# Performance work log

Measured on AMD Instinct MI355X. Metric: run time of the kernel, lower is better.

## Reference

```python
import jax, jax.numpy as jnp
import numpy as np

INPUT_DIM = 6
HIDDEN = 128


def neighbor_mean(x, adj):
    # x: [B,N,F], adj: [B,N,N]; node i averages itself + neighbors (adj>0)
    mask = (adj > 0).astype(x.dtype)  # [B,N,N]
    s = jnp.einsum('bij,bjf->bif', mask, x) + x  # sum neighbors + self
    cnt = mask.sum(-1) + 1.0  # [B,N]
    return s / cnt[..., None]


def lstm_scan(x, Wi, Wh, bi, bh, reverse=False):
    # x: [B,T,F]; Wi: [4H,F]; Wh: [4H,H]; gate order i,f,g,o (torch)
    B, T, F = x.shape
    H = Wh.shape[1]
    xw = jnp.einsum('btf,gf->btg', x, Wi) + bi + bh  # [B,T,4H]
    def step(carry, xt):
        h, c = carry
        z = xt + h @ Wh.T  # [B,4H]
        i, f, g, o = jnp.split(z, 4, axis=-1)
        i = jax.nn.sigmoid(i); f = jax.nn.sigmoid(f)
        g = jnp.tanh(g); o = jax.nn.sigmoid(o)
        c = f * c + i * g
        h = o * jnp.tanh(c)
        return (h, c), h
    init = (jnp.zeros((B, H), x.dtype), jnp.zeros((B, H), x.dtype))
    xs = jnp.swapaxes(xw, 0, 1)  # [T,B,4H]
    (hT, cT), hs = jax.lax.scan(step, init, xs, reverse=reverse)
    return hT


def setup_inputs():
    key = jax.random.key(0)
    ks = jax.random.split(key, 12)
    B, N = 4096, 64
    inp = {
        'device_idx': jax.random.uniform(ks[0], (B,), jnp.float32),
        'matrix': jax.random.uniform(ks[1], (B, N, N), jnp.float32),
        'features': jax.random.normal(ks[2], (B, N, INPUT_DIM), jnp.float32),
    }
    s = 1.0 / np.sqrt(HIDDEN)
    def u(k, shape):
        return jax.random.uniform(k, shape, jnp.float32, -s, s)
    inp['Wi_f'] = u(ks[3], (4 * HIDDEN, INPUT_DIM))
    inp['Wh_f'] = u(ks[4], (4 * HIDDEN, HIDDEN))
    inp['bi_f'] = u(ks[5], (4 * HIDDEN,))
    inp['bh_f'] = u(ks[6], (4 * HIDDEN,))
    inp['Wi_b'] = u(ks[7], (4 * HIDDEN, INPUT_DIM))
    inp['Wh_b'] = u(ks[8], (4 * HIDDEN, HIDDEN))
    inp['bi_b'] = u(ks[9], (4 * HIDDEN,))
    inp['bh_b'] = u(ks[10], (4 * HIDDEN,))
    inp['fc_w'] = u(ks[11], (1, 2 * HIDDEN + 1))
    inp['fc_b'] = jnp.zeros((1,), jnp.float32)
    return inp


def reference(device_idx, matrix, features, Wi_f, Wh_f, bi_f, bh_f, Wi_b, Wh_b, bi_b, bh_b, fc_w, fc_b):
    upd = neighbor_mean(features, matrix)  # [B,N,6]
    h_fwd = lstm_scan(upd, Wi_f, Wh_f, bi_f, bh_f, reverse=False)  # [B,H]
    h_bwd = lstm_scan(upd, Wi_b, Wh_b, bi_b, bh_b, reverse=True)   # [B,H]
    hn = jnp.concatenate([h_fwd, h_bwd], axis=1)  # [B,2H]
    final = jnp.concatenate([device_idx[:, None], hn], axis=1)  # [B,2H+1]
    y = final @ fc_w.T + fc_b
    return y.reshape(-1)
```

## Files before the change

kernel.cpp:

```cpp
#include <hip/hip_runtime.h>
#include <hip/hip_bf16.h>

#define B_TOTAL 4096
#define LOG2E 1.44269504088896f

typedef short short8 __attribute__((ext_vector_type(8)));
typedef float f32x4 __attribute__((ext_vector_type(4)));
typedef int   i32x4 __attribute__((ext_vector_type(4)));

__device__ __forceinline__ unsigned short rne_bf16(float x) {
    unsigned int u = __float_as_uint(x);
    unsigned int r = (u + 0x7fffu + ((u >> 16) & 1u)) >> 16;
    return (unsigned short)r;
}
__device__ __forceinline__ unsigned int cvt2bf(float lo, float hi) {
    unsigned int r;
    asm("v_cvt_pk_bf16_f32 %0, %1, %2" : "=v"(r) : "v"(lo), "v"(hi));
    return r;
}

__global__ __launch_bounds__(256) void k_neighbor_mean(
    const float* __restrict__ matrix,
    const float* __restrict__ features,
    float* __restrict__ upd)
{
    __shared__ float adj[64][65];
    __shared__ float fx[64][6];
    const int b = blockIdx.x;
    const int tid = threadIdx.x;
    const float* mb_ = matrix + (size_t)b * 4096;
    for (int idx = tid; idx < 4096; idx += 256) adj[idx >> 6][idx & 63] = mb_[idx];
    const float* fb = features + (size_t)b * 384;
    for (int idx = tid; idx < 384; idx += 256) fx[idx / 6][idx % 6] = fb[idx];
    __syncthreads();
    if (tid < 64) {
        const int i = tid;
        float s0=0,s1=0,s2=0,s3=0,s4=0,s5=0,cnt=0;
        for (int j = 0; j < 64; j++) {
            float m = adj[i][j] > 0.0f ? 1.0f : 0.0f;
            cnt += m;
            s0 += m*fx[j][0]; s1 += m*fx[j][1]; s2 += m*fx[j][2];
            s3 += m*fx[j][3]; s4 += m*fx[j][4]; s5 += m*fx[j][5];
        }
        const float inv = 1.0f / (cnt + 1.0f);
        float* o = upd + (size_t)b * 384 + i * 6;
        o[0]=(s0+fx[i][0])*inv; o[1]=(s1+fx[i][1])*inv; o[2]=(s2+fx[i][2])*inv;
        o[3]=(s3+fx[i][3])*inv; o[4]=(s4+fx[i][4])*inv; o[5]=(s5+fx[i][5])*inv;
    }
}

__global__ __launch_bounds__(256) void k_wprep5(
    const float* __restrict__ Wi_f, const float* __restrict__ Wh_f,
    const float* __restrict__ bi_f, const float* __restrict__ bh_f,
    const float* __restrict__ Wi_b, const float* __restrict__ Wh_b,
    const float* __restrict__ bi_b, const float* __restrict__ bh_b,
    signed char* __restrict__ Wd1, signed char* __restrict__ Wd2,
    unsigned short* __restrict__ AwU, float* __restrict__ BqO)
{
    const int idx = blockIdx.x * 256 + threadIdx.x;
    if (idx < 131072) {
        const int dir = idx >> 16;
        const int r = idx & 65535;
        const int mtg = r >> 11;
        const int kc  = (r >> 10) & 1;
        const int l   = (r >> 4) & 63;
        const int e   = r & 15;
        const int n = mtg * 16 + (l & 15);
        const int j = ((n & 3) << 7) + (n >> 2);
        const int ks = kc * 64 + 16 * (l >> 4) + e;
        const int hu = 8 * (ks >> 3) + 4 * (ks & 1) + ((ks & 7) >> 1);
        const float w = (dir ? Wh_b : Wh_f)[j * 128 + hu];
        const float a = w * (512.0f * LOG2E);
        const float r1 = rintf(a);
        Wd1[idx] = (signed char)(int)r1;
        Wd2[idx] = (signed char)(int)rintf((a - r1) * 128.0f);
    } else if (idx < 163840) {
        const int i2 = idx - 131072;
        const int dir = i2 >> 14;
        const int r = i2 & 16383;
        const int mtg = r >> 9, l = (r >> 3) & 63, e = r & 7;
        const int n = mtg * 16 + (l & 15);
        const int j = ((n & 3) << 7) + (n >> 2);
        const float sc = ((n & 3) == 2) ? 2.0f * LOG2E : LOG2E;
        float w = 0.0f;
        if ((l >> 4) == 0 && e < 6) w = (dir ? Wi_b : Wi_f)[j * 6 + e] * sc;
        AwU[i2] = rne_bf16(w);
    } else if (idx < 164864) {
        const int i2 = idx - 163840;
        const int dir = i2 >> 9;
        const int n = i2 & 511;
        const int j = ((n & 3) << 7) + (n >> 2);
        const float sc = ((n & 3) == 2) ? 2.0f * LOG2E : LOG2E;
        BqO[i2] = ((dir ? bi_b : bi_f)[j] + (dir ? bh_b : bh_f)[j]) * sc;
    }
}

__global__ __launch_bounds__(1024) void k_lstm8(
    const float* __restrict__ upd,
    const signed char* __restrict__ Wd1,
    const signed char* __restrict__ Wd2,
    const unsigned short* __restrict__ AwU,
    const float* __restrict__ Bq,
    float* __restrict__ hout)
{
    __shared__ i32x4 HsV[2048];
    __shared__ i32x4 UsV[2048];
    char* Hb = (char*)HsV;
    char* Ub = (char*)UsV;
    const int tid  = threadIdx.x;
    const int wave = tid >> 6;
    const int lane = tid & 63;
    const int dir  = blockIdx.y;
    const int b0   = blockIdx.x * 32;
    const int l15  = lane & 15;
    const int lhi  = lane >> 4;
    const int hu0  = 8 * wave + lhi, hu1 = hu0 + 4;

    i32x4 wd1[2][2], wd2[2][2];
    short8 awu[2];
    f32x4 bias[2];
    #pragma unroll
    for (int mt = 0; mt < 2; mt++) {
        const int mtg = 2 * wave + mt;
        #pragma unroll
        for (int kc = 0; kc < 2; kc++) {
            wd1[mt][kc] = *(const i32x4*)(Wd1 + dir * 65536 + mtg * 2048 + kc * 1024 + lane * 16);
            wd2[mt][kc] = *(const i32x4*)(Wd2 + dir * 65536 + mtg * 2048 + kc * 1024 + lane * 16);
        }
        awu[mt]  = *(const short8*)(AwU + dir * 16384 + mtg * 512 + lane * 8);
        bias[mt] = *(const f32x4*)(Bq + dir * 512 + mtg * 16 + 4 * lhi);
    }

    for (int i = tid; i < 2048; i += 1024) {
        const int t = i >> 5, b = i & 31;
        const float2* p = (const float2*)(upd + (size_t)(b0 + b) * 384 + t * 6);
        const float2 a0 = p[0], a1 = p[1], a2 = p[2];
        i32x4 v;
        v[0] = (int)cvt2bf(a0.x, a0.y);
        v[1] = (int)cvt2bf(a1.x, a1.y);
        v[2] = (int)cvt2bf(a2.x, a2.y);
        v[3] = 0;
        *(i32x4*)(Ub + (b >> 4) * 16384 + t * 256 + (b & 15) * 16) = v;
    }
    for (int i = tid; i < 8192; i += 1024) ((int*)Hb)[i] = 0;

    int ra[2], wa[2];
    #pragma unroll
    for (int g = 0; g < 2; g++) {
        ra[g] = g * 16384 + 4096 + l15 * 144 + lhi * 16;
        wa[g] = g * 16384 + l15 * 144 + 8 * wave + 2 * lhi;
    }
    float cs[2][2] = {{0.0f, 0.0f}, {0.0f, 0.0f}};
    f32x4 Ua[2][2];
    i32x4 Aa[2][2], Ba[2][2];
    __syncthreads();

    const i32x4 zi = {0, 0, 0, 0};

    {
        const int tt = dir ? 63 : 0;
        const short8 fu = *(const short8*)(Ub + tt * 256 + l15 * 16);
        const i32x4 h1k0 = *(const i32x4*)(Hb + ra[0]);
        const i32x4 h1k1 = *(const i32x4*)(Hb + ra[0] + 64);
        const i32x4 h2k0 = *(const i32x4*)(Hb + ra[0] + 8192);
        const i32x4 h2k1 = *(const i32x4*)(Hb + ra[0] + 8256);
        ra[0] ^= 0x1000;
        #pragma unroll
        for (int mt = 0; mt < 2; mt++) {
            Ua[0][mt] = __builtin_amdgcn_mfma_f32_16x16x32_bf16(awu[mt], fu, bias[mt], 0, 0, 0);
            i32x4 a = __builtin_amdgcn_mfma_i32_16x16x64_i8(wd1[mt][0], h1k0, zi, 0, 0, 0);
            a = __builtin_amdgcn_mfma_i32_16x16x64_i8(wd1[mt][1], h1k1, a, 0, 0, 0);
            i32x4 b = __builtin_amdgcn_mfma_i32_16x16x64_i8(wd1[mt][0], h2k0, zi, 0, 0, 0);
            b = __builtin_amdgcn_mfma_i32_16x16x64_i8(wd1[mt][1], h2k1, b, 0, 0, 0);
            b = __builtin_amdgcn_mfma_i32_16x16x64_i8(wd2[mt][0], h1k0, b, 0, 0, 0);
            b = __builtin_amdgcn_mfma_i32_16x16x64_i8(wd2[mt][1], h1k1, b, 0, 0, 0);
            Aa[0][mt] = a; Ba[0][mt] = b;
        }
    }

    #pragma unroll 2
    for (int iv = 0; iv < 128; ++iv) {
        const int gc = iv & 1;
        const int sc = iv >> 1;

        float z[2][4];
        #pragma unroll
        for (int mt = 0; mt < 2; mt++)
            #pragma unroll
            for (int i = 0; i < 4; i++) {
                const int T = (Aa[gc][mt][i] << 7) + Ba[gc][mt][i];
                z[mt][i] = fmaf((float)T, (i == 2) ? 0x1p-21f : 0x1p-22f, Ua[gc][mt][i]);
            }

        if (iv < 127) {
            const int gi = gc ^ 1;
            const int si = (iv + 1) >> 1;
            const int tt = dir ? (63 - si) : si;
            const short8 fu = *(const short8*)(Ub + gi * 16384 + tt * 256 + l15 * 16);
            const i32x4 h1k0 = *(const i32x4*)(Hb + ra[gi]);
            const i32x4 h1k1 = *(const i32x4*)(Hb + ra[gi] + 64);
            const i32x4 h2k0 = *(const i32x4*)(Hb + ra[gi] + 8192);
            const i32x4 h2k1 = *(const i32x4*)(Hb + ra[gi] + 8256);
            ra[gi] ^= 0x1000;
            __builtin_amdgcn_s_setprio(1);
            #pragma unroll
            for (int mt = 0; mt < 2; mt++) {
                Ua[gi][mt] = __builtin_amdgcn_mfma_f32_16x16x32_bf16(awu[mt], fu, bias[mt], 0, 0, 0);
                i32x4 a = __builtin_amdgcn_mfma_i32_16x16x64_i8(wd1[mt][0], h1k0, zi, 0, 0, 0);
                a = __builtin_amdgcn_mfma_i32_16x16x64_i8(wd1[mt][1], h1k1, a, 0, 0, 0);
                i32x4 b = __builtin_amdgcn_mfma_i32_16x16x64_i8(wd1[mt][0], h2k0, zi, 0, 0, 0);
                b = __builtin_amdgcn_mfma_i32_16x16x64_i8(wd1[mt][1], h2k1, b, 0, 0, 0);
                b = __builtin_amdgcn_mfma_i32_16x16x64_i8(wd2[mt][0], h1k0, b, 0, 0, 0);
                b = __builtin_amdgcn_mfma_i32_16x16x64_i8(wd2[mt][1], h1k1, b, 0, 0, 0);
                Aa[gi][mt] = a; Ba[gi][mt] = b;
            }
            __builtin_amdgcn_s_setprio(0);
        }

        float ig[2], fg[2], gg[2], og[2], Dq[2], hh[2];
        #pragma unroll
        for (int mt = 0; mt < 2; mt++) {
            const float D0 = 1.0f + __builtin_amdgcn_exp2f(-z[mt][0]);
            const float D1 = 1.0f + __builtin_amdgcn_exp2f(-z[mt][1]);
            const float D2 = 1.0f + __builtin_amdgcn_exp2f( z[mt][2]);
            const float D3 = 1.0f + __builtin_amdgcn_exp2f(-z[mt][3]);
            const float P2 = D0 * D1, P3 = P2 * D2, P4 = P3 * D3;
            const float r  = __builtin_amdgcn_rcpf(P4);
            const float Q2 = D3 * D2, Q3 = Q2 * D1;
            ig[mt] = r * Q3;
            fg[mt] = (r * Q2) * D0;
            og[mt] = r * P3;
            gg[mt] = fmaf(-2.0f, (r * P2) * D3, 1.0f);
        }
        #pragma unroll
        for (int mt = 0; mt < 2; mt++) {
            cs[gc][mt] = fmaf(fg[mt], cs[gc][mt], ig[mt] * gg[mt]);
            Dq[mt] = 1.0f + __builtin_amdgcn_exp2f(fminf(cs[gc][mt] * (2.0f * LOG2E), 30.0f));
        }
        const float rq = __builtin_amdgcn_rcpf(Dq[0] * Dq[1]);
        hh[0] = og[0] * fmaf(-2.0f, rq * Dq[1], 1.0f);
        hh[1] = og[1] * fmaf(-2.0f, rq * Dq[0], 1.0f);

        if (sc < 63) {
            int d1[2], d2[2];
            #pragma unroll
            for (int mt = 0; mt < 2; mt++) {
                const int t = __float_as_int(fmaf(hh[mt], 8192.0f, 12582912.0f)) - 0x4B400000;
                d1[mt] = (t + 64) >> 7;
                d2[mt] = t - (d1[mt] << 7);
            }
            *(unsigned short*)(Hb + wa[gc]) =
                (unsigned short)__builtin_amdgcn_perm((unsigned)d1[1], (unsigned)d1[0], 0x0400);
            *(unsigned short*)(Hb + wa[gc] + 8192) =
                (unsigned short)__builtin_amdgcn_perm((unsigned)d2[1], (unsigned)d2[0], 0x0400);
        } else {
            float* o = hout + ((size_t)dir * B_TOTAL + b0 + gc * 16 + l15) * 128;
            o[hu0] = hh[0];
            o[hu1] = hh[1];
        }
        wa[gc] ^= 0x1000;
        __syncthreads();
    }
}

__global__ __launch_bounds__(256) void k_final(
    const float* __restrict__ hout,
    const float* __restrict__ device_idx,
    const float* __restrict__ fc_w,
    const float* __restrict__ fc_b,
    float* __restrict__ y)
{
    const int wave = threadIdx.x >> 6;
    const int lane = threadIdx.x & 63;
    const int b = blockIdx.x * 4 + wave;
    const float* hf = hout + (size_t)b * 128;
    const float* hb = hout + ((size_t)B_TOTAL + b) * 128;
    float p = fc_w[1 + lane]        * hf[lane]
            + fc_w[1 + 64 + lane]   * hf[64 + lane]
            + fc_w[129 + lane]      * hb[lane]
            + fc_w[129 + 64 + lane] * hb[64 + lane];
    #pragma unroll
    for (int off = 32; off; off >>= 1) p += __shfl_xor(p, off, 64);
    if (lane == 0) y[b] = p + fc_w[0] * device_idx[b] + fc_b[0];
}

extern "C" void kernel_launch(void* const* d_in, const int* in_sizes, int n_in,
                              void* d_out, int out_size, void* d_ws, size_t ws_size,
                              hipStream_t stream) {
    const float* device_idx = (const float*)d_in[0];
    const float* matrix     = (const float*)d_in[1];
    const float* features   = (const float*)d_in[2];
    const float* Wi_f = (const float*)d_in[3];
    const float* Wh_f = (const float*)d_in[4];
    const float* bi_f = (const float*)d_in[5];
    const float* bh_f = (const float*)d_in[6];
    const float* Wi_b = (const float*)d_in[7];
    const float* Wh_b = (const float*)d_in[8];
    const float* bi_b = (const float*)d_in[9];
    const float* bh_b = (const float*)d_in[10];
    const float* fc_w = (const float*)d_in[11];
    const float* fc_b = (const float*)d_in[12];
    float* out = (float*)d_out;

    float* ws = (float*)d_ws;
    float*          upd  = ws;
    signed char*    Wd1  = (signed char*)(ws + 1572864);
    signed char*    Wd2  = (signed char*)(ws + 1605632);
    unsigned short* AwU  = (unsigned short*)(ws + 1638400);
    float*          Bq   = ws + 1654784;
    float*          hout = ws + 1655808;

    hipLaunchKernelGGL(k_neighbor_mean, dim3(B_TOTAL), dim3(256), 0, stream,
                       matrix, features, upd);
    hipLaunchKernelGGL(k_wprep5, dim3(644), dim3(256), 0, stream,
                       Wi_f, Wh_f, bi_f, bh_f, Wi_b, Wh_b, bi_b, bh_b,
                       Wd1, Wd2, AwU, Bq);
    hipLaunchKernelGGL(k_lstm8, dim3(B_TOTAL / 32, 2), dim3(1024), 0, stream,
                       upd, Wd1, Wd2, AwU, Bq, hout);
    hipLaunchKernelGGL(k_final, dim3(B_TOTAL / 4), dim3(256), 0, stream,
                       hout, device_idx, fc_w, fc_b, out);
}
```

Measured before the change: 163.2 us.

## Process 16 batch rows per LSTM block without two-group interleave, use packed float2 math

The LSTM kernel previously gave each 1024-thread block 32 batch rows as two 16-row groups. It interleaved them so one group's MFMA work overlapped the other group's gate math. Now each block handles 16 rows in a simple per-step loop, which doubles the grid (512 blocks) and halves LDS use. The gate and cell math is also rewritten in f32x2 vectors to encourage packed FP32 ops. This trades the intra-block MFMA/VALU overlap for more blocks per CU and lower register and LDS pressure, relying on the hardware to overlap work across blocks instead.

```diff
diff --git a/kernel.cpp b/kernel.cpp
--- a/kernel.cpp
+++ b/kernel.cpp
@@ -6,6 +6,7 @@
 
 typedef short short8 __attribute__((ext_vector_type(8)));
 typedef float f32x4 __attribute__((ext_vector_type(4)));
+typedef float f32x2 __attribute__((ext_vector_type(2)));
 typedef int   i32x4 __attribute__((ext_vector_type(4)));
 
 __device__ __forceinline__ unsigned short rne_bf16(float x) {
@@ -18,6 +19,7 @@
     asm("v_cvt_pk_bf16_f32 %0, %1, %2" : "=v"(r) : "v"(lo), "v"(hi));
     return r;
 }
+__device__ __forceinline__ f32x2 v2(float x) { f32x2 r; r[0] = x; r[1] = x; return r; }
 
 __global__ __launch_bounds__(256) void k_neighbor_mean(
     const float* __restrict__ matrix,
@@ -95,7 +97,7 @@
     }
 }
 
-__global__ __launch_bounds__(1024) void k_lstm8(
+__global__ __launch_bounds__(1024) void k_lstm10(
     const float* __restrict__ upd,
     const signed char* __restrict__ Wd1,
     const signed char* __restrict__ Wd2,
@@ -103,15 +105,15 @@
     const float* __restrict__ Bq,
     float* __restrict__ hout)
 {
-    __shared__ i32x4 HsV[2048];
-    __shared__ i32x4 UsV[2048];
+    __shared__ i32x4 HsV[1024];
+    __shared__ i32x4 UsV[1024];
     char* Hb = (char*)HsV;
     char* Ub = (char*)UsV;
     const int tid  = threadIdx.x;
     const int wave = tid >> 6;
     const int lane = tid & 63;
     const int dir  = blockIdx.y;
-    const int b0   = blockIdx.x * 32;
+    const int b0   = blockIdx.x * 16;
     const int l15  = lane & 15;
     const int lhi  = lane >> 4;
     const int hu0  = 8 * wave + lhi, hu1 = hu0 + 4;
@@ -131,8 +133,8 @@
         bias[mt] = *(const f32x4*)(Bq + dir * 512 + mtg * 16 + 4 * lhi);
     }
 
-    for (int i = tid; i < 2048; i += 1024) {
-        const int t = i >> 5, b = i & 31;
+    {
+        const int t = tid >> 4, b = tid & 15;
         const float2* p = (const float2*)(upd + (size_t)(b0 + b) * 384 + t * 6);
         const float2 a0 = p[0], a1 = p[1], a2 = p[2];
         i32x4 v;
@@ -140,125 +142,103 @@
         v[1] = (int)cvt2bf(a1.x, a1.y);
         v[2] = (int)cvt2bf(a2.x, a2.y);
         v[3] = 0;
-        *(i32x4*)(Ub + (b >> 4) * 16384 + t * 256 + (b & 15) * 16) = v;
-    }
-    for (int i = tid; i < 8192; i += 1024) ((int*)Hb)[i] = 0;
-
-    int ra[2], wa[2];
-    #pragma unroll
-    for (int g = 0; g < 2; g++) {
-        ra[g] = g * 16384 + 4096 + l15 * 144 + lhi * 16;
-        wa[g] = g * 16384 + l15 * 144 + 8 * wave + 2 * lhi;
-    }
-    float cs[2][2] = {{0.0f, 0.0f}, {0.0f, 0.0f}};
-    f32x4 Ua[2][2];
-    i32x4 Aa[2][2], Ba[2][2];
+        *(i32x4*)(Ub + t * 256 + b * 16) = v;
+    }
+    {
+        i32x4 z4; z4[0] = 0; z4[1] = 0; z4[2] = 0; z4[3] = 0;
+        *(i32x4*)(Hb + tid * 16) = z4;
+    }
+
+    int ra = 4096 + l15 * 144 + lhi * 16;
+    int wa = l15 * 144 + 8 * wave + 2 * lhi;
+    f32x2 cs = v2(0.0f);
     __syncthreads();
 
     const i32x4 zi = {0, 0, 0, 0};
-
-    {
-        const int tt = dir ? 63 : 0;
-        const short8 fu = *(const short8*)(Ub + tt * 256 + l15 * 16);
-        const i32x4 h1k0 = *(const i32x4*)(Hb + ra[0]);
-        const i32x4 h1k1 = *(const i32x4*)(Hb + ra[0] + 64);
-        const i32x4 h2k0 = *(const i32x4*)(Hb + ra[0] + 8192);
-        const i32x4 h2k1 = *(const i32x4*)(Hb + ra[0] + 8256);
-        ra[0] ^= 0x1000;
+    const f32x2 one2 = v2(1.0f);
+    const f32x2 two2 = v2(2.0f);
+
+    #pragma unroll 1
+    for (int s = 0; s < 64; ++s) {
+        const int t = dir ? (63 - s) : s;
+        const short8 fu = *(const short8*)(Ub + t * 256 + l15 * 16);
+
+        const i32x4 h1k0 = *(const i32x4*)(Hb + ra);
+        const i32x4 h1k1 = *(const i32x4*)(Hb + ra + 64);
+        const i32x4 h2k0 = *(const i32x4*)(Hb + ra + 8192);
+        const i32x4 h2k1 = *(const i32x4*)(Hb + ra + 8256);
+        f32x4 Ua[2];
+        i32x4 Aa[2], Ba[2];
+        __builtin_amdgcn_s_setprio(1);
         #pragma unroll
         for (int mt = 0; mt < 2; mt++) {
-            Ua[0][mt] = __builtin_amdgcn_mfma_f32_16x16x32_bf16(awu[mt], fu, bias[mt], 0, 0, 0);
+            Ua[mt] = __builtin_amdgcn_mfma_f32_16x16x32_bf16(awu[mt], fu, bias[mt], 0, 0, 0);
             i32x4 a = __builtin_amdgcn_mfma_i32_16x16x64_i8(wd1[mt][0], h1k0, zi, 0, 0, 0);
             a = __builtin_amdgcn_mfma_i32_16x16x64_i8(wd1[mt][1], h1k1, a, 0, 0, 0);
             i32x4 b = __builtin_amdgcn_mfma_i32_16x16x64_i8(wd1[mt][0], h2k0, zi, 0, 0, 0);
             b = __builtin_amdgcn_mfma_i32_16x16x64_i8(wd1[mt][1], h2k1, b, 0, 0, 0);
             b = __builtin_amdgcn_mfma_i32_16x16x64_i8(wd2[mt][0], h1k0, b, 0, 0, 0);
             b = __builtin_amdgcn_mfma_i32_16x16x64_i8(wd2[mt][1], h1k1, b, 0, 0, 0);
-            Aa[0][mt] = a; Ba[0][mt] = b;
-        }
-    }
-
-    #pragma unroll 2
-    for (int iv = 0; iv < 128; ++iv) {
-        const int gc = iv & 1;
-        const int sc = iv >> 1;
-
-        float z[2][4];
+            Aa[mt] = a; Ba[mt] = b;
+        }
+        __builtin_amdgcn_s_setprio(0);
+        ra ^= 0x1000;
+
+        f32x2 zv[4];
         #pragma unroll
-        for (int mt = 0; mt < 2; mt++)
-            #pragma unroll
-            for (int i = 0; i < 4; i++) {
-                const int T = (Aa[gc][mt][i] << 7) + Ba[gc][mt][i];
-                z[mt][i] = fmaf((float)T, (i == 2) ? 0x1p-21f : 0x1p-22f, Ua[gc][mt][i]);
-            }
-
-        if (iv < 127) {
-            const int gi = gc ^ 1;
-            const int si = (iv + 1) >> 1;
-            const int tt = dir ? (63 - si) : si;
-            const short8 fu = *(const short8*)(Ub + gi * 16384 + tt * 256 + l15 * 16);
-            const i32x4 h1k0 = *(const i32x4*)(Hb + ra[gi]);
-            const i32x4 h1k1 = *(const i32x4*)(Hb + ra[gi] + 64);
-            const i32x4 h2k0 = *(const i32x4*)(Hb + ra[gi] + 8192);
-            const i32x4 h2k1 = *(const i32x4*)(Hb + ra[gi] + 8256);
-            ra[gi] ^= 0x1000;
-            __builtin_amdgcn_s_setprio(1);
-            #pragma unroll
-            for (int mt = 0; mt < 2; mt++) {
-                Ua[gi][mt] = __builtin_amdgcn_mfma_f32_16x16x32_bf16(awu[mt], fu, bias[mt], 0, 0, 0);
-                i32x4 a = __builtin_amdgcn_mfma_i32_16x16x64_i8(wd1[mt][0], h1k0, zi, 0, 0, 0);
-                a = __builtin_amdgcn_mfma_i32_16x16x64_i8(wd1[mt][1], h1k1, a, 0, 0, 0);
-                i32x4 b = __builtin_amdgcn_mfma_i32_16x16x64_i8(wd1[mt][0], h2k0, zi, 0, 0, 0);
-                b = __builtin_amdgcn_mfma_i32_16x16x64_i8(wd1[mt][1], h2k1, b, 0, 0, 0);
-                b = __builtin_amdgcn_mfma_i32_16x16x64_i8(wd2[mt][0], h1k0, b, 0, 0, 0);
-                b = __builtin_amdgcn_mfma_i32_16x16x64_i8(wd2[mt][1], h1k1, b, 0, 0, 0);
-                Aa[gi][mt] = a; Ba[gi][mt] = b;
-            }
-            __builtin_amdgcn_s_setprio(0);
-        }
-
-        float ig[2], fg[2], gg[2], og[2], Dq[2], hh[2];
-        #pragma unroll
-        for (int mt = 0; mt < 2; mt++) {
-            const float D0 = 1.0f + __builtin_amdgcn_exp2f(-z[mt][0]);
-            const float D1 = 1.0f + __builtin_amdgcn_exp2f(-z[mt][1]);
-            const float D2 = 1.0f + __builtin_amdgcn_exp2f( z[mt][2]);
-            const float D3 = 1.0f + __builtin_amdgcn_exp2f(-z[mt][3]);
-            const float P2 = D0 * D1, P3 = P2 * D2, P4 = P3 * D3;
-            const float r  = __builtin_amdgcn_rcpf(P4);
-            const float Q2 = D3 * D2, Q3 = Q2 * D1;
-            ig[mt] = r * Q3;
-            fg[mt] = (r * Q2) * D0;
-            og[mt] = r * P3;
-            gg[mt] = fmaf(-2.0f, (r * P2) * D3, 1.0f);
-        }
-        #pragma unroll
-        for (int mt = 0; mt < 2; mt++) {
-            cs[gc][mt] = fmaf(fg[mt], cs[gc][mt], ig[mt] * gg[mt]);
-            Dq[mt] = 1.0f + __builtin_amdgcn_exp2f(fminf(cs[gc][mt] * (2.0f * LOG2E), 30.0f));
-        }
-        const float rq = __builtin_amdgcn_rcpf(Dq[0] * Dq[1]);
-        hh[0] = og[0] * fmaf(-2.0f, rq * Dq[1], 1.0f);
-        hh[1] = og[1] * fmaf(-2.0f, rq * Dq[0], 1.0f);
-
-        if (sc < 63) {
-            int d1[2], d2[2];
-            #pragma unroll
-            for (int mt = 0; mt < 2; mt++) {
-                const int t = __float_as_int(fmaf(hh[mt], 8192.0f, 12582912.0f)) - 0x4B400000;
-                d1[mt] = (t + 64) >> 7;
-                d2[mt] = t - (d1[mt] << 7);
-            }
-            *(unsigned short*)(Hb + wa[gc]) =
-                (unsigned short)__builtin_amdgcn_perm((unsigned)d1[1], (unsigned)d1[0], 0x0400);
-            *(unsigned short*)(Hb + wa[gc] + 8192) =
-                (unsigned short)__builtin_amdgcn_perm((unsigned)d2[1], (unsigned)d2[0], 0x0400);
+        for (int i = 0; i < 4; i++) {
+            const int T0 = (Aa[0][i] << 7) + Ba[0][i];
+            const int T1 = (Aa[1][i] << 7) + Ba[1][i];
+            const float sc = (i == 2) ? 0x1p-21f : 0x1p-22f;
+            f32x2 zf;
+            zf[0] = fmaf((float)T0, sc, Ua[0][i]);
+            zf[1] = fmaf((float)T1, sc, Ua[1][i]);
+            zv[i] = zf;
+        }
+        f32x2 E0, E1, E2, E3;
+        E0[0] = __builtin_amdgcn_exp2f(-zv[0][0]); E0[1] = __builtin_amdgcn_exp2f(-zv[0][1]);
+        E1[0] = __builtin_amdgcn_exp2f(-zv[1][0]); E1[1] = __builtin_amdgcn_exp2f(-zv[1][1]);
+        E2[0] = __builtin_amdgcn_exp2f( zv[2][0]); E2[1] = __builtin_amdgcn_exp2f( zv[2][1]);
+        E3[0] = __builtin_amdgcn_exp2f(-zv[3][0]); E3[1] = __builtin_amdgcn_exp2f(-zv[3][1]);
+        const f32x2 D0 = E0 + one2;
+        const f32x2 D1 = E1 + one2;
+        const f32x2 D2 = E2 + one2;
+        const f32x2 D3 = E3 + one2;
+        const f32x2 P2 = D0 * D1, P3 = P2 * D2, P4 = P3 * D3;
+        f32x2 rr;
+        rr[0] = __builtin_amdgcn_rcpf(P4[0]);
+        rr[1] = __builtin_amdgcn_rcpf(P4[1]);
+        const f32x2 Q2 = D3 * D2, Q3 = Q2 * D1;
+        const f32x2 ig = rr * Q3;
+        const f32x2 fg = rr * Q2 * D0;
+        const f32x2 og = rr * P3;
+        const f32x2 gg = one2 - two2 * (rr * P2 * D3);
+        cs = fg * cs + ig * gg;
+        const float aa0 = fminf(cs[0] * (2.0f * LOG2E), 30.0f);
+        const float aa1 = fminf(cs[1] * (2.0f * LOG2E), 30.0f);
+        const float Dq0 = 1.0f + __builtin_amdgcn_exp2f(aa0);
+        const float Dq1 = 1.0f + __builtin_amdgcn_exp2f(aa1);
+        const float rq = __builtin_amdgcn_rcpf(Dq0 * Dq1);
+        const float hh0 = og[0] * fmaf(-2.0f, rq * Dq1, 1.0f);
+        const float hh1 = og[1] * fmaf(-2.0f, rq * Dq0, 1.0f);
+
+        if (s < 63) {
+            const int t0 = __float_as_int(fmaf(hh0, 8192.0f, 12582912.0f)) - 0x4B400000;
+            const int t1 = __float_as_int(fmaf(hh1, 8192.0f, 12582912.0f)) - 0x4B400000;
+            const int d10 = (t0 + 64) >> 7;
+            const int d20 = t0 - (d10 << 7);
+            const int d11 = (t1 + 64) >> 7;
+            const int d21 = t1 - (d11 << 7);
+            *(unsigned short*)(Hb + wa) =
+                (unsigned short)__builtin_amdgcn_perm((unsigned)d11, (unsigned)d10, 0x0400);
+            *(unsigned short*)(Hb + wa + 8192) =
+                (unsigned short)__builtin_amdgcn_perm((unsigned)d21, (unsigned)d20, 0x0400);
         } else {
-            float* o = hout + ((size_t)dir * B_TOTAL + b0 + gc * 16 + l15) * 128;
-            o[hu0] = hh[0];
-            o[hu1] = hh[1];
-        }
-        wa[gc] ^= 0x1000;
+            float* o = hout + ((size_t)dir * B_TOTAL + b0 + l15) * 128;
+            o[hu0] = hh0;
+            o[hu1] = hh1;
+        }
+        wa ^= 0x1000;
         __syncthreads();
     }
 }
@@ -315,7 +295,7 @@
     hipLaunchKernelGGL(k_wprep5, dim3(644), dim3(256), 0, stream,
                        Wi_f, Wh_f, bi_f, bh_f, Wi_b, Wh_b, bi_b, bh_b,
                        Wd1, Wd2, AwU, Bq);
-    hipLaunchKernelGGL(k_lstm8, dim3(B_TOTAL / 32, 2), dim3(1024), 0, stream,
+    hipLaunchKernelGGL(k_lstm10, dim3(B_TOTAL / 16, 2), dim3(1024), 0, stream,
                        upd, Wd1, Wd2, AwU, Bq, hout);
     hipLaunchKernelGGL(k_final, dim3(B_TOTAL / 4), dim3(256), 0, stream,
                        hout, device_idx, fc_w, fc_b, out);
```

Result: slower. 169.5 us (+3.9%).
